# Performance work log

Measured on AMD Instinct MI355X. Metric: run time of the kernel, lower is better.

## Reference

```python
import jax, jax.numpy as jnp
import numpy as np


def setup_inputs() -> dict:
    key = jax.random.key(0)
    k1, k2, k3 = jax.random.split(key, 3)
    N, S, D = 8, 2048, 1024
    x = jax.random.normal(k1, (N, S, D), dtype=jnp.float32)
    # kaiming_normal_ on a (1,1,D) tensor: std = sqrt(2 / fan_in) with fan_in = D
    std = np.sqrt(2.0 / D).astype(np.float32)
    w_lhs = jax.random.normal(k2, (1, 1, D), dtype=jnp.float32) * std
    w_rhs = jax.random.normal(k3, (1, 1, D), dtype=jnp.float32) * std
    return {"x": x, "w_lhs": w_lhs, "w_rhs": w_rhs}


def reference(x, w_lhs, w_rhs):
    # x: (N, S, D); w_lhs/w_rhs: (1, 1, D) broadcast elementwise scales
    lhs = x * w_lhs                       # (N, S, D)
    rhs = x * w_rhs                       # (N, S, D)
    scores = jnp.einsum('nsd,ntd->nst', lhs, rhs)  # (N, S, S), no 1/sqrt(d) scaling
    attn = jax.nn.softmax(scores, axis=2)
    return jnp.einsum('nst,ntd->nsd', attn, x)     # (N, S, D)
```

## Files before the change

### kernel.cpp

```cpp
#include <hip/hip_runtime.h>
#include <hip/hip_bf16.h>
#include <stdint.h>

typedef unsigned short u16;
typedef unsigned int u32;
typedef __attribute__((ext_vector_type(8))) short bf16x8;
typedef __attribute__((ext_vector_type(4))) float f32x4;

#define S_DIM 2048
#define D_DIM 1024

__device__ __forceinline__ u16 f2bf(float f) {
  u32 u = __float_as_uint(f);
  u += 0x7FFFu + ((u >> 16) & 1u);
  return (u16)(u >> 16);
}

typedef const __attribute__((address_space(1))) u32* gas1p;
typedef __attribute__((address_space(3))) u32* las3p;

__device__ __forceinline__ void gload_lds16(const void* g, void* l) {
  __builtin_amdgcn_global_load_lds((gas1p)g, (las3p)l, 16, 0, 0);
}

__device__ __forceinline__ void mfma16(f32x4& c, bf16x8 a, bf16x8 b) {
  c = __builtin_amdgcn_mfma_f32_16x16x32_bf16(a, b, c, 0, 0, 0);
}

__global__ __launch_bounds__(256) void prep_kernel(
    const float* __restrict__ x, const float* __restrict__ wl,
    const float* __restrict__ wr, u16* __restrict__ Qb, u16* __restrict__ Kb,
    u16* __restrict__ Vt, float* __restrict__ lsum, int batch0) {
  const int S = S_DIM, D = D_DIM;
  int nz = blockIdx.z;
  const float* xb = x + (size_t)(batch0 + nz) * S * D;
  u16* Qn = Qb + (size_t)nz * S * D;
  u16* Kn = Kb + (size_t)nz * S * D;
  u16* Vn = Vt + (size_t)nz * D * S;
  int t0 = blockIdx.x * 64;
  int d0 = blockIdx.y * 64;
  int tid = threadIdx.x;
  int rl = tid >> 4;
  int cl = (tid & 15) << 2;

  if (blockIdx.y == 0 && tid < 64) lsum[(size_t)nz * S + t0 + tid] = 0.0f;

  __shared__ u16 ldsT[64][68];

  float4 a = *(const float4*)(wl + d0 + cl);
  float4 b = *(const float4*)(wr + d0 + cl);
  float wv0 = a.x * b.x, wv1 = a.y * b.y, wv2 = a.z * b.z, wv3 = a.w * b.w;

#pragma unroll
  for (int p = 0; p < 4; ++p) {
    int r = p * 16 + rl;
    float4 xv = *(const float4*)(xb + (size_t)(t0 + r) * D + d0 + cl);
    u16 q0 = f2bf(xv.x), q1 = f2bf(xv.y), q2 = f2bf(xv.z), q3 = f2bf(xv.w);
    u16 k0 = f2bf(xv.x * wv0), k1 = f2bf(xv.y * wv1);
    u16 k2 = f2bf(xv.z * wv2), k3 = f2bf(xv.w * wv3);
    uint2 qpk;
    qpk.x = (u32)q0 | ((u32)q1 << 16);
    qpk.y = (u32)q2 | ((u32)q3 << 16);
    *(uint2*)(Qn + (size_t)(t0 + r) * D + d0 + cl) = qpk;
    uint2 kpk;
    kpk.x = (u32)k0 | ((u32)k1 << 16);
    kpk.y = (u32)k2 | ((u32)k3 << 16);
    *(uint2*)(Kn + (size_t)(t0 + r) * D + d0 + cl) = kpk;
    ldsT[cl + 0][r] = q0;
    ldsT[cl + 1][r] = q1;
    ldsT[cl + 2][r] = q2;
    ldsT[cl + 3][r] = q3;
  }
  __syncthreads();
#pragma unroll
  for (int p = 0; p < 4; ++p) {
    int dr = p * 16 + rl;
    u16 v0 = ldsT[dr][cl + 0], v1 = ldsT[dr][cl + 1];
    u16 v2 = ldsT[dr][cl + 2], v3 = ldsT[dr][cl + 3];
    uint2 pk;
    pk.x = (u32)v0 | ((u32)v1 << 16);
    pk.y = (u32)v2 | ((u32)v3 << 16);
    *(uint2*)(Vn + (size_t)(d0 + dr) * S + t0 + cl) = pk;
  }
}

__device__ __forceinline__ void gemm_main(const u16* __restrict__ A,
                                          const u16* __restrict__ B, int m0,
                                          int n0, int ldk, int NT, char* cl,
                                          int tid, f32x4 (&acc)[8][4]) {
  int lane = tid & 63, w = tid >> 6;
  int lk = lane & 15, g8 = lane >> 4, l7 = lane & 7;
  int wr = w >> 2, wc = w & 3;
  int sA0 = (wr * 128 + lk) * 128;
  int sB0 = (wc * 64 + lk) * 128 + 32768;
  int sx0 = (g8 ^ l7) << 4;
  int sx1 = ((4 + g8) ^ l7) << 4;
  int r8 = lane >> 3;
  int kel = (l7 ^ r8) << 3;
  const u16* gAs = A + (size_t)(m0 + w * 16 + r8) * ldk + kel;
  const u16* gBs = B + (size_t)(n0 + w * 16 + r8) * ldk + kel;
  char* dA = cl + w * 2048;
  char* dB = cl + 32768 + w * 2048;

#define STG_A(kt_, h_, b_)                                                  \
  {                                                                         \
    const u16* g_ = gAs + (size_t)(kt_)*64 + (size_t)(h_)*128 * ldk;        \
    char* d_ = dA + (b_)*65536 + (h_)*16384;                                \
    gload_lds16(g_, d_);                                                    \
    gload_lds16(g_ + 8 * (size_t)ldk, d_ + 1024);                           \
  }
#define STG_B(kt_, h_, b_)                                                  \
  {                                                                         \
    const u16* g_ = gBs + (size_t)(kt_)*64 + (size_t)(h_)*128 * ldk;        \
    char* d_ = dB + (b_)*65536 + (h_)*16384;                                \
    gload_lds16(g_, d_);                                                    \
    gload_lds16(g_ + 8 * (size_t)ldk, d_ + 1024);                           \
  }

  STG_A(0, 0, 0);
  STG_A(0, 1, 0);
  STG_B(0, 0, 0);
  STG_B(0, 1, 0);
  STG_A(1, 0, 1);
  asm volatile("s_waitcnt vmcnt(2)");
  __builtin_amdgcn_s_barrier();

  bf16x8 af0[4][2], af1[4][2], bfr[2][2];

#pragma unroll 1
  for (int kt = 0; kt < NT; ++kt) {
    int b = kt & 1, nb = b ^ 1;
    int bo = b * 65536;
#pragma unroll
    for (int m = 0; m < 4; ++m) {
      af0[m][0] = *(const bf16x8*)(cl + bo + sA0 + m * 2048 + sx0);
      af0[m][1] = *(const bf16x8*)(cl + bo + sA0 + m * 2048 + sx1);
    }
#pragma unroll
    for (int n = 0; n < 2; ++n) {
      bfr[n][0] = *(const bf16x8*)(cl + bo + sB0 + n * 2048 + sx0);
      bfr[n][1] = *(const bf16x8*)(cl + bo + sB0 + n * 2048 + sx1);
    }
    if (kt + 1 < NT) STG_A(kt + 1, 1, nb);
    __builtin_amdgcn_s_barrier();
    asm volatile("s_waitcnt lgkmcnt(0)");
    __builtin_amdgcn_s_setprio(1);
#pragma unroll
    for (int m = 0; m < 4; ++m)
#pragma unroll
      for (int n = 0; n < 2; ++n) {
        mfma16(acc[m][n], af0[m][0], bfr[n][0]);
        mfma16(acc[m][n], af0[m][1], bfr[n][1]);
      }
    __builtin_amdgcn_s_setprio(0);
    __builtin_amdgcn_s_barrier();
#pragma unroll
    for (int m = 0; m < 4; ++m) {
      af1[m][0] = *(const bf16x8*)(cl + bo + sA0 + (m + 4) * 2048 + sx0);
      af1[m][1] = *(const bf16x8*)(cl + bo + sA0 + (m + 4) * 2048 + sx1);
    }
    if (kt + 1 < NT) STG_B(kt + 1, 0, nb);
    __builtin_amdgcn_s_barrier();
    asm volatile("s_waitcnt lgkmcnt(0)");
    __builtin_amdgcn_s_setprio(1);
#pragma unroll
    for (int m = 0; m < 4; ++m)
#pragma unroll
      for (int n = 0; n < 2; ++n) {
        mfma16(acc[m + 4][n], af1[m][0], bfr[n][0]);
        mfma16(acc[m + 4][n], af1[m][1], bfr[n][1]);
      }
    __builtin_amdgcn_s_setprio(0);
    __builtin_amdgcn_s_barrier();
#pragma unroll
    for (int n = 0; n < 2; ++n) {
      bfr[n][0] = *(const bf16x8*)(cl + bo + sB0 + (n + 2) * 2048 + sx0);
      bfr[n][1] = *(const bf16x8*)(cl + bo + sB0 + (n + 2) * 2048 + sx1);
    }
    if (kt + 1 < NT) STG_B(kt + 1, 1, nb);
    __builtin_amdgcn_s_barrier();
    asm volatile("s_waitcnt lgkmcnt(0)");
    __builtin_amdgcn_s_setprio(1);
#pragma unroll
    for (int m = 0; m < 4; ++m)
#pragma unroll
      for (int n = 0; n < 2; ++n) {
        mfma16(acc[m][n + 2], af0[m][0], bfr[n][0]);
        mfma16(acc[m][n + 2], af0[m][1], bfr[n][1]);
      }
    __builtin_amdgcn_s_setprio(0);
    __builtin_amdgcn_s_barrier();
    if (kt + 2 < NT) STG_A(kt + 2, 0, b);
    __builtin_amdgcn_s_barrier();
    asm volatile("s_waitcnt lgkmcnt(0)");
    __builtin_amdgcn_s_setprio(1);
#pragma unroll
    for (int m = 0; m < 4; ++m)
#pragma unroll
      for (int n = 0; n < 2; ++n) {
        mfma16(acc[m + 4][n + 2], af1[m][0], bfr[n][0]);
        mfma16(acc[m + 4][n + 2], af1[m][1], bfr[n][1]);
      }
    __builtin_amdgcn_s_setprio(0);
    if (kt + 2 < NT) {
      asm volatile("s_waitcnt vmcnt(2)");
    } else {
      asm volatile("s_waitcnt vmcnt(0)");
    }
    __builtin_amdgcn_s_barrier();
  }
#undef STG_A
#undef STG_B
}

__global__ __launch_bounds__(512, 2) void qk_exp_kernel(
    const u16* __restrict__ Qb, const u16* __restrict__ Kb,
    u16* __restrict__ P, float* __restrict__ lsum) {
  const int S = S_DIM, D = D_DIM;
  int nz = blockIdx.z;
  const u16* A = Qb + (size_t)nz * S * D;
  const u16* B = Kb + (size_t)nz * S * D;
  u16* C = P + (size_t)nz * S * S;
  float* lrow = lsum + (size_t)nz * S;

  int m0 = blockIdx.x * 256;
  int n0 = blockIdx.y * 256;
  int tid = threadIdx.x;

  __shared__ __align__(16) u16 lds[65536];
  f32x4 acc[8][4] = {};
  gemm_main(A, B, m0, n0, D, D / 64, (char*)lds, tid, acc);

  int lane = tid & 63, w = tid >> 6;
  int lk = lane & 15, g8 = lane >> 4;
  int wr = w >> 2, wc = w & 3;
  int rr = g8 << 2;
#pragma unroll
  for (int m = 0; m < 8; ++m) {
    int rowb = m0 + wr * 128 + m * 16 + rr;
    float rs[4] = {0.f, 0.f, 0.f, 0.f};
#pragma unroll
    for (int n = 0; n < 4; ++n) {
#pragma unroll
      for (int r = 0; r < 4; ++r) {
        float e = __expf(fminf(acc[m][n][r], 30.0f));
        rs[r] += e;
        C[(size_t)(rowb + r) * S + n0 + wc * 64 + n * 16 + lk] = f2bf(e);
      }
    }
#pragma unroll
    for (int d = 1; d < 16; d <<= 1) {
      rs[0] += __shfl_xor(rs[0], d);
      rs[1] += __shfl_xor(rs[1], d);
      rs[2] += __shfl_xor(rs[2], d);
      rs[3] += __shfl_xor(rs[3], d);
    }
    if (lk == 0) {
#pragma unroll
      for (int r = 0; r < 4; ++r) atomicAdd(&lrow[rowb + r], rs[r]);
    }
  }
}

__global__ __launch_bounds__(512, 2) void pv_kernel(
    const u16* __restrict__ P, const u16* __restrict__ Vt,
    const float* __restrict__ lsum, float* __restrict__ out) {
  const int S = S_DIM, D = D_DIM;
  int nz = blockIdx.z;
  const u16* A = P + (size_t)nz * S * S;
  const u16* B = Vt + (size_t)nz * D * S;
  const float* lrow = lsum + (size_t)nz * S;
  float* Cn = out + (size_t)nz * S * D;

  int m0 = blockIdx.x * 256;
  int n0 = blockIdx.y * 256;
  int tid = threadIdx.x;

  __shared__ __align__(16) u16 lds[65536];
  f32x4 acc[8][4] = {};
  gemm_main(A, B, m0, n0, S, S / 64, (char*)lds, tid, acc);

  int lane = tid & 63, w = tid >> 6;
  int lk = lane & 15, g8 = lane >> 4;
  int wr = w >> 2, wc = w & 3;
  int rr = g8 << 2;
#pragma unroll
  for (int m = 0; m < 8; ++m) {
    int rowb = m0 + wr * 128 + m * 16 + rr;
#pragma unroll
    for (int r = 0; r < 4; ++r) {
      float inv = __fdividef(1.0f, lrow[rowb + r]);
      float* cp = Cn + (size_t)(rowb + r) * D + n0 + wc * 64 + lk;
      cp[0] = acc[m][0][r] * inv;
      cp[16] = acc[m][1][r] * inv;
      cp[32] = acc[m][2][r] * inv;
      cp[48] = acc[m][3][r] * inv;
    }
  }
}

extern "C" void kernel_launch(void* const* d_in, const int* in_sizes, int n_in,
                              void* d_out, int out_size, void* d_ws,
                              size_t ws_size, hipStream_t stream) {
  const float* x = (const float*)d_in[0];
  const float* wl = (const float*)d_in[1];
  const float* wr = (const float*)d_in[2];
  float* out = (float*)d_out;
  const int N = 8, S = S_DIM, D = D_DIM;
  const size_t szQ = (size_t)S * D;
  const size_t szP = (size_t)S * S;

  int g = 8;
  while (g > 1) {
    size_t need = (size_t)g * (3 * szQ * 2 + szP * 2 + (size_t)S * 4);
    if (need <= ws_size) break;
    g >>= 1;
  }

  for (int b0 = 0; b0 < N; b0 += g) {
    u16* Qb = (u16*)d_ws;
    u16* Kb = Qb + (size_t)g * szQ;
    u16* Vt = Kb + (size_t)g * szQ;
    u16* Pp = Vt + (size_t)g * szQ;
    float* lsum = (float*)(Pp + (size_t)g * szP);
    hipLaunchKernelGGL(prep_kernel, dim3(S / 64, D / 64, g), dim3(256), 0,
                       stream, x, wl, wr, Qb, Kb, Vt, lsum, b0);
    hipLaunchKernelGGL(qk_exp_kernel, dim3(S / 256, S / 256, g), dim3(512), 0,
                       stream, Qb, Kb, Pp, lsum);
    hipLaunchKernelGGL(pv_kernel, dim3(S / 256, D / 256, g), dim3(512), 0,
                       stream, Pp, Vt, lsum, out + (size_t)b0 * S * D);
  }
}
```

Before: 270.7 us.

## Simplify GEMM main loop to single-stage prefetch and swizzle block mapping for XCDs

Replaces the four-phase interleaved load/MFMA schedule with a simpler loop. Each iteration prefetches the entire next K-tile into the other LDS buffer, loads all A/B fragments, then runs all MFMAs, with one vmcnt wait and barrier per iteration. It also remaps block IDs so that blocks sharing the same batch and tiles land on the same XCD (mod-8 swizzle), aiming for better L2 reuse. The simpler schedule raises register pressure from holding all fragments at once and loses the fine-grained overlap of LDS reads with compute.

```diff
diff --git a/kernel.cpp b/kernel.cpp
--- a/kernel.cpp
+++ b/kernel.cpp
@@ -102,129 +102,80 @@
   char* dA = cl + w * 2048;
   char* dB = cl + 32768 + w * 2048;
 
-#define STG_A(kt_, h_, b_)                                                  \
-  {                                                                         \
-    const u16* g_ = gAs + (size_t)(kt_)*64 + (size_t)(h_)*128 * ldk;        \
-    char* d_ = dA + (b_)*65536 + (h_)*16384;                                \
-    gload_lds16(g_, d_);                                                    \
-    gload_lds16(g_ + 8 * (size_t)ldk, d_ + 1024);                           \
-  }
-#define STG_B(kt_, h_, b_)                                                  \
-  {                                                                         \
-    const u16* g_ = gBs + (size_t)(kt_)*64 + (size_t)(h_)*128 * ldk;        \
-    char* d_ = dB + (b_)*65536 + (h_)*16384;                                \
-    gload_lds16(g_, d_);                                                    \
-    gload_lds16(g_ + 8 * (size_t)ldk, d_ + 1024);                           \
-  }
-
-  STG_A(0, 0, 0);
-  STG_A(0, 1, 0);
-  STG_B(0, 0, 0);
-  STG_B(0, 1, 0);
-  STG_A(1, 0, 1);
-  asm volatile("s_waitcnt vmcnt(2)");
+#define STG_ALL(kt_, b_)                                   \
+  {                                                        \
+    const u16* ga_ = gAs + (size_t)(kt_)*64;               \
+    const u16* gb_ = gBs + (size_t)(kt_)*64;               \
+    char* da_ = dA + (b_)*65536;                           \
+    char* db_ = dB + (b_)*65536;                           \
+    gload_lds16(ga_, da_);                                 \
+    gload_lds16(ga_ + 8 * (size_t)ldk, da_ + 1024);        \
+    gload_lds16(ga_ + 128 * (size_t)ldk, da_ + 16384);     \
+    gload_lds16(ga_ + 136 * (size_t)ldk, da_ + 17408);     \
+    gload_lds16(gb_, db_);                                 \
+    gload_lds16(gb_ + 8 * (size_t)ldk, db_ + 1024);        \
+    gload_lds16(gb_ + 128 * (size_t)ldk, db_ + 16384);     \
+    gload_lds16(gb_ + 136 * (size_t)ldk, db_ + 17408);     \
+  }
+
+  STG_ALL(0, 0);
+  asm volatile("s_waitcnt vmcnt(0)");
   __builtin_amdgcn_s_barrier();
-
-  bf16x8 af0[4][2], af1[4][2], bfr[2][2];
 
 #pragma unroll 1
   for (int kt = 0; kt < NT; ++kt) {
-    int b = kt & 1, nb = b ^ 1;
+    int b = kt & 1;
     int bo = b * 65536;
-#pragma unroll
-    for (int m = 0; m < 4; ++m) {
-      af0[m][0] = *(const bf16x8*)(cl + bo + sA0 + m * 2048 + sx0);
-      af0[m][1] = *(const bf16x8*)(cl + bo + sA0 + m * 2048 + sx1);
-    }
-#pragma unroll
-    for (int n = 0; n < 2; ++n) {
-      bfr[n][0] = *(const bf16x8*)(cl + bo + sB0 + n * 2048 + sx0);
-      bfr[n][1] = *(const bf16x8*)(cl + bo + sB0 + n * 2048 + sx1);
-    }
-    if (kt + 1 < NT) STG_A(kt + 1, 1, nb);
+    if (kt + 1 < NT) STG_ALL(kt + 1, b ^ 1);
+
+    bf16x8 a0[8], a1[8], b0[4], b1[4];
+#pragma unroll
+    for (int m = 0; m < 8; ++m)
+      a0[m] = *(const bf16x8*)(cl + bo + sA0 + m * 2048 + sx0);
+#pragma unroll
+    for (int n = 0; n < 4; ++n)
+      b0[n] = *(const bf16x8*)(cl + bo + sB0 + n * 2048 + sx0);
+#pragma unroll
+    for (int m = 0; m < 8; ++m)
+      a1[m] = *(const bf16x8*)(cl + bo + sA0 + m * 2048 + sx1);
+#pragma unroll
+    for (int n = 0; n < 4; ++n)
+      b1[n] = *(const bf16x8*)(cl + bo + sB0 + n * 2048 + sx1);
+
+    __builtin_amdgcn_s_setprio(1);
+#pragma unroll
+    for (int m = 0; m < 8; ++m)
+#pragma unroll
+      for (int n = 0; n < 4; ++n) mfma16(acc[m][n], a0[m], b0[n]);
+#pragma unroll
+    for (int m = 0; m < 8; ++m)
+#pragma unroll
+      for (int n = 0; n < 4; ++n) mfma16(acc[m][n], a1[m], b1[n]);
+    __builtin_amdgcn_s_setprio(0);
+
+    asm volatile("s_waitcnt vmcnt(0)");
     __builtin_amdgcn_s_barrier();
-    asm volatile("s_waitcnt lgkmcnt(0)");
-    __builtin_amdgcn_s_setprio(1);
-#pragma unroll
-    for (int m = 0; m < 4; ++m)
-#pragma unroll
-      for (int n = 0; n < 2; ++n) {
-        mfma16(acc[m][n], af0[m][0], bfr[n][0]);
-        mfma16(acc[m][n], af0[m][1], bfr[n][1]);
-      }
-    __builtin_amdgcn_s_setprio(0);
-    __builtin_amdgcn_s_barrier();
-#pragma unroll
-    for (int m = 0; m < 4; ++m) {
-      af1[m][0] = *(const bf16x8*)(cl + bo + sA0 + (m + 4) * 2048 + sx0);
-      af1[m][1] = *(const bf16x8*)(cl + bo + sA0 + (m + 4) * 2048 + sx1);
-    }
-    if (kt + 1 < NT) STG_B(kt + 1, 0, nb);
-    __builtin_amdgcn_s_barrier();
-    asm volatile("s_waitcnt lgkmcnt(0)");
-    __builtin_amdgcn_s_setprio(1);
-#pragma unroll
-    for (int m = 0; m < 4; ++m)
-#pragma unroll
-      for (int n = 0; n < 2; ++n) {
-        mfma16(acc[m + 4][n], af1[m][0], bfr[n][0]);
-        mfma16(acc[m + 4][n], af1[m][1], bfr[n][1]);
-      }
-    __builtin_amdgcn_s_setprio(0);
-    __builtin_amdgcn_s_barrier();
-#pragma unroll
-    for (int n = 0; n < 2; ++n) {
-      bfr[n][0] = *(const bf16x8*)(cl + bo + sB0 + (n + 2) * 2048 + sx0);
-      bfr[n][1] = *(const bf16x8*)(cl + bo + sB0 + (n + 2) * 2048 + sx1);
-    }
-    if (kt + 1 < NT) STG_B(kt + 1, 1, nb);
-    __builtin_amdgcn_s_barrier();
-    asm volatile("s_waitcnt lgkmcnt(0)");
-    __builtin_amdgcn_s_setprio(1);
-#pragma unroll
-    for (int m = 0; m < 4; ++m)
-#pragma unroll
-      for (int n = 0; n < 2; ++n) {
-        mfma16(acc[m][n + 2], af0[m][0], bfr[n][0]);
-        mfma16(acc[m][n + 2], af0[m][1], bfr[n][1]);
-      }
-    __builtin_amdgcn_s_setprio(0);
-    __builtin_amdgcn_s_barrier();
-    if (kt + 2 < NT) STG_A(kt + 2, 0, b);
-    __builtin_amdgcn_s_barrier();
-    asm volatile("s_waitcnt lgkmcnt(0)");
-    __builtin_amdgcn_s_setprio(1);
-#pragma unroll
-    for (int m = 0; m < 4; ++m)
-#pragma unroll
-      for (int n = 0; n < 2; ++n) {
-        mfma16(acc[m + 4][n + 2], af1[m][0], bfr[n][0]);
-        mfma16(acc[m + 4][n + 2], af1[m][1], bfr[n][1]);
-      }
-    __builtin_amdgcn_s_setprio(0);
-    if (kt + 2 < NT) {
-      asm volatile("s_waitcnt vmcnt(2)");
-    } else {
-      asm volatile("s_waitcnt vmcnt(0)");
-    }
-    __builtin_amdgcn_s_barrier();
-  }
-#undef STG_A
-#undef STG_B
+  }
+#undef STG_ALL
 }
 
 __global__ __launch_bounds__(512, 2) void qk_exp_kernel(
     const u16* __restrict__ Qb, const u16* __restrict__ Kb,
     u16* __restrict__ P, float* __restrict__ lsum) {
   const int S = S_DIM, D = D_DIM;
-  int nz = blockIdx.z;
-  const u16* A = Qb + (size_t)nz * S * D;
-  const u16* B = Kb + (size_t)nz * S * D;
-  u16* C = P + (size_t)nz * S * S;
-  float* lrow = lsum + (size_t)nz * S;
-
-  int m0 = blockIdx.x * 256;
-  int n0 = blockIdx.y * 256;
+  int gz = gridDim.z;
+  int lid = blockIdx.x + (blockIdx.y << 3) + (blockIdx.z << 6);
+  int cpx = gz << 3;
+  int swz = (lid & 7) * cpx + (lid >> 3);
+  int bx = swz & 7, by = (swz >> 3) & 7, bz = swz >> 6;
+
+  const u16* A = Qb + (size_t)bz * S * D;
+  const u16* B = Kb + (size_t)bz * S * D;
+  u16* C = P + (size_t)bz * S * S;
+  float* lrow = lsum + (size_t)bz * S;
+
+  int m0 = bx * 256;
+  int n0 = by * 256;
   int tid = threadIdx.x;
 
   __shared__ __align__(16) u16 lds[65536];
@@ -266,14 +217,19 @@
     const u16* __restrict__ P, const u16* __restrict__ Vt,
     const float* __restrict__ lsum, float* __restrict__ out) {
   const int S = S_DIM, D = D_DIM;
-  int nz = blockIdx.z;
-  const u16* A = P + (size_t)nz * S * S;
-  const u16* B = Vt + (size_t)nz * D * S;
-  const float* lrow = lsum + (size_t)nz * S;
-  float* Cn = out + (size_t)nz * S * D;
-
-  int m0 = blockIdx.x * 256;
-  int n0 = blockIdx.y * 256;
+  int gz = gridDim.z;
+  int lid = blockIdx.x + (blockIdx.y << 3) + (blockIdx.z << 5);
+  int cpx = gz << 2;
+  int swz = (lid & 7) * cpx + (lid >> 3);
+  int bx = swz & 7, by = (swz >> 3) & 3, bz = swz >> 5;
+
+  const u16* A = P + (size_t)bz * S * S;
+  const u16* B = Vt + (size_t)bz * D * S;
+  const float* lrow = lsum + (size_t)bz * S;
+  float* Cn = out + (size_t)bz * S * D;
+
+  int m0 = bx * 256;
+  int n0 = by * 256;
   int tid = threadIdx.x;
 
   __shared__ __align__(16) u16 lds[65536];
```

Result: faster. 255.3 us (-5.7%).
